# Kernel tuning notes

Measured on AMD Instinct MI355X. Metric: run time of the kernel, lower is better.

## Reference

```python
import jax, jax.numpy as jnp
import numpy as np
import math

B, N, D, H = 2, 64, 256, 8
DK = D // H


def setup_inputs() -> dict:
    key = jax.random.key(0)
    ks = jax.random.split(key, 12)
    s = 1.0 / math.sqrt(D)
    inp = {
        "state": jax.random.normal(ks[0], (B, N, N, D), dtype=jnp.float32),
        "mask": jnp.zeros((B, N, N, N), dtype=bool),
        "W_lk": jax.random.normal(ks[1], (D, D), dtype=jnp.float32) * s,
        "b_lk": jnp.zeros((D,), dtype=jnp.float32),
        "W_rk": jax.random.normal(ks[2], (D, D), dtype=jnp.float32) * s,
        "b_rk": jnp.zeros((D,), dtype=jnp.float32),
        "W_lv": jax.random.normal(ks[3], (D, D), dtype=jnp.float32) * s,
        "b_lv": jnp.zeros((D,), dtype=jnp.float32),
        "W_rv": jax.random.normal(ks[4], (D, D), dtype=jnp.float32) * s,
        "b_rv": jnp.zeros((D,), dtype=jnp.float32),
        "W_o": jax.random.normal(ks[5], (D, D), dtype=jnp.float32) * s,
        "b_o": jnp.zeros((D,), dtype=jnp.float32),
    }
    return inp


def _proj(x, W, b):
    # torch nn.Linear: x @ W.T + b, then view to heads
    y = jnp.einsum('bxyd,ed->bxye', x, W) + b
    return y.reshape(B, N, N, H, DK)


def reference(state, mask, W_lk, b_lk, W_rk, b_rk, W_lv, b_lv, W_rv, b_rv, W_o, b_o):
    left_k = _proj(state, W_lk, b_lk)   # [B,N,N,H,DK]
    right_k = _proj(state, W_rk, b_rk)
    left_v = _proj(state, W_lv, b_lv)
    right_v = _proj(state, W_rv, b_rv)

    # triangle-style scores over node triples (x, a, y): [B,N,N,N,H]
    scores = jnp.einsum('bxahd,bayhd->bxayh', left_k, right_k) / math.sqrt(DK)
    scores = jnp.where(mask[..., None], jnp.float32(-1000.0), scores)
    att = jax.nn.softmax(scores, axis=2)  # softmax over intermediate node a

    # val[b,x,a,y,h,d] = left_v[b,x,a,h,d] * right_v[b,a,y,h,d] (materialized as in torch)
    val = jnp.einsum('bxahd,bayhd->bxayhd', left_v, right_v)
    x = jnp.einsum('bxayh,bxayhd->bxyhd', att, val)  # sum over a
    x = x.reshape(B, N, N, D)
    return jnp.einsum('bxyd,ed->bxye', x, W_o) + b_o
```

## Files before the change

### kernel.cpp

```cpp
#include <hip/hip_runtime.h>

#define B 2
#define N 64
#define D 256
#define H 8
#define DK 32
#define M (B * N * N)

typedef __attribute__((ext_vector_type(8))) short bf16x8;
typedef __attribute__((ext_vector_type(4))) float f32x4;

#define OFF_LK 0
#define OFF_RK 256
#define OFF_LV 512
#define OFF_RV 768

__device__ __forceinline__ ushort f2b(float f) {
    union { float f; unsigned u; } v; v.f = f;
    unsigned r = v.u + 0x7fffu + ((v.u >> 16) & 1u);
    return (ushort)(r >> 16);
}
__device__ __forceinline__ float b2f(ushort u) {
    union { unsigned u; float f; } v; v.u = ((unsigned)u) << 16; return v.f;
}
__device__ __forceinline__ void cvt8(float4 raw, float* f) {
    const ushort* s = (const ushort*)&raw;
#pragma unroll
    for (int j = 0; j < 8; ++j) f[j] = b2f(s[j]);
}

__device__ __forceinline__ void glds16(const ushort* g, ushort* l) {
    __builtin_amdgcn_global_load_lds(
        (const __attribute__((address_space(1))) unsigned int*)g,
        (__attribute__((address_space(3))) unsigned int*)l, 16, 0, 0);
}

__global__ __launch_bounds__(256) void cast_all(const float* __restrict__ state,
                                                const float* __restrict__ W_lk, const float* __restrict__ W_rk,
                                                const float* __restrict__ W_lv, const float* __restrict__ W_rv,
                                                const float* __restrict__ W_o,
                                                const float* __restrict__ b_lk, const float* __restrict__ b_rk,
                                                const float* __restrict__ b_lv, const float* __restrict__ b_rv,
                                                const float* __restrict__ b_o,
                                                ushort* __restrict__ state_bf,
                                                ushort* __restrict__ Wcat,
                                                float* __restrict__ bias_cat) {
    const int gid = blockIdx.x * 256 + threadIdx.x;
    const float* Ws[5] = {W_lk, W_rk, W_lv, W_rv, W_o};
    const float* bs[5] = {b_lk, b_rk, b_lv, b_rv, b_o};

    if (gid < 1280) bias_cat[gid] = bs[gid >> 8][gid & 255];

    if (gid < 524288) {
        float4 v = *(const float4*)&state[(size_t)gid * 4];
        ushort4 o = {f2b(v.x), f2b(v.y), f2b(v.z), f2b(v.w)};
        *(ushort4*)&state_bf[(size_t)gid * 4] = o;
    } else {
        int u = gid - 524288;
        int row = u >> 6;
        int k4 = (u & 63) * 4;
        const float* W = Ws[row >> 8];
        float4 v = *(const float4*)&W[(size_t)(row & 255) * 256 + k4];
        ushort4 o = {f2b(v.x), f2b(v.y), f2b(v.z), f2b(v.w)};
        *(ushort4*)&Wcat[(size_t)row * 256 + k4] = o;
    }
}

template <int BF16OUT>
__global__ __launch_bounds__(256) void gemm_mfma(const ushort* __restrict__ A,
                                                 const ushort* __restrict__ Bw,
                                                 const float* __restrict__ bias,
                                                 void* __restrict__ Cv, int ldc) {
    __shared__ __align__(16) ushort As[128 * 32];
    __shared__ __align__(16) ushort Bs[128 * 32];
    const int tid = threadIdx.x;
    const int lane = tid & 63;
    const int wave = tid >> 6;
    const int wm = (wave & 1) * 64;
    const int wn = (wave >> 1) * 64;
    const int row0 = blockIdx.x * 128;
    const int col0 = blockIdx.y * 128;

    const int lr = lane >> 2;
    const int lkq = (lane & 3) * 8;

    const ushort* gA0 = A + (size_t)(row0 + wave * 32 + lr) * 256 + lkq;
    const ushort* gA1 = gA0 + 16 * 256;
    const ushort* gB0 = Bw + (size_t)(col0 + wave * 32 + lr) * 256 + lkq;
    const ushort* gB1 = gB0 + 16 * 256;
    ushort* lA0 = &As[(wave * 32) * 32];
    ushort* lA1 = &As[(wave * 32 + 16) * 32];
    ushort* lB0 = &Bs[(wave * 32) * 32];
    ushort* lB1 = &Bs[(wave * 32 + 16) * 32];

    const int fr = lane & 15;
    const int fk = (lane >> 4) * 8;

    f32x4 acc[4][4] = {};

    for (int k0 = 0; k0 < 256; k0 += 32) {
        __syncthreads();
        glds16(gA0 + k0, lA0);
        glds16(gA1 + k0, lA1);
        glds16(gB0 + k0, lB0);
        glds16(gB1 + k0, lB1);
        __syncthreads();

        bf16x8 af[4], bf[4];
#pragma unroll
        for (int i = 0; i < 4; ++i)
            af[i] = *(const bf16x8*)&As[(wm + i * 16 + fr) * 32 + fk];
#pragma unroll
        for (int j = 0; j < 4; ++j)
            bf[j] = *(const bf16x8*)&Bs[(wn + j * 16 + fr) * 32 + fk];
#pragma unroll
        for (int i = 0; i < 4; ++i)
#pragma unroll
            for (int j = 0; j < 4; ++j)
                acc[i][j] = __builtin_amdgcn_mfma_f32_16x16x32_bf16(af[i], bf[j], acc[i][j], 0, 0, 0);
    }

#pragma unroll
    for (int j = 0; j < 4; ++j) {
        const int col = col0 + wn + j * 16 + (lane & 15);
        const float bv = bias[col];
#pragma unroll
        for (int i = 0; i < 4; ++i) {
            const int rbase = row0 + wm + i * 16 + (lane >> 4) * 4;
#pragma unroll
            for (int r = 0; r < 4; ++r) {
                float o = acc[i][j][r] + bv;
                if (BF16OUT) ((ushort*)Cv)[(size_t)(rbase + r) * ldc + col] = f2b(o);
                else ((float*)Cv)[(size_t)(rbase + r) * ldc + col] = o;
            }
        }
    }
}

__global__ __launch_bounds__(256) void fused_attn(const ushort* __restrict__ P,
                                                  const unsigned char* __restrict__ mask,
                                                  ushort* __restrict__ xbuf) {
    __shared__ __align__(16) ushort LKs[8 * 16 * 40];
    __shared__ __align__(16) ushort RKs[8 * 16 * 40];
    __shared__ __align__(16) float2 LVs[8 * 16 * 18];
    __shared__ __align__(16) float2 RVs[8 * 16 * 18];
    __shared__ __align__(16) float atts[8 * 16 * 20];
    __shared__ __align__(16) unsigned char masks[16 * 8 * 16];
    __shared__ float mstate[16 * 20];
    __shared__ float lstate[16 * 20];
    __shared__ float alphas[16 * 20];

    const int bh = blockIdx.z;
    const int b = bh >> 3, h = bh & 7;
    const int x0 = blockIdx.x * 16, y0 = blockIdx.y * 16;
    const int tid = threadIdx.x;
    const int lane = tid & 63, wave = tid >> 6;

    const int xg = tid >> 6, yg = (tid >> 4) & 3, dp = tid & 15;
    const int sx = tid >> 4, sy = tid & 15;

    mstate[sx * 20 + sy] = -3.0e38f;
    lstate[sx * 20 + sy] = 0.0f;

    float2 acc[4][4] = {};
    const float scale = 0.17677669529663687f;

    for (int ac = 0; ac < N; ac += 8) {
        __syncthreads();
        {
            const int r = tid >> 1, q = tid & 1;
            const int xs = r >> 3, as = r & 7;
            const int ar = r >> 4, yr = r & 15;
            {
                const ushort* s = &P[(((size_t)b * N + x0 + xs) * N + ac + as) * 1024 + OFF_LK + h * DK + q * 16];
                *(float4*)&LKs[(as * 16 + xs) * 40 + q * 16]     = *(const float4*)&s[0];
                *(float4*)&LKs[(as * 16 + xs) * 40 + q * 16 + 8] = *(const float4*)&s[8];
            }
            {
                const ushort* s = &P[(((size_t)b * N + ac + ar) * N + y0 + yr) * 1024 + OFF_RK + h * DK + q * 16];
                *(float4*)&RKs[(ar * 16 + yr) * 40 + q * 16]     = *(const float4*)&s[0];
                *(float4*)&RKs[(ar * 16 + yr) * 40 + q * 16 + 8] = *(const float4*)&s[8];
            }
            float f[16];
            {
                const ushort* s = &P[(((size_t)b * N + x0 + xs) * N + ac + as) * 1024 + OFF_LV + h * DK + q * 16];
                cvt8(*(const float4*)&s[0], f);
                cvt8(*(const float4*)&s[8], f + 8);
#pragma unroll
                for (int m2 = 0; m2 < 8; ++m2)
                    LVs[(as * 16 + q * 8 + m2) * 18 + xs] = make_float2(f[2 * m2], f[2 * m2 + 1]);
            }
            {
                const ushort* s = &P[(((size_t)b * N + ac + ar) * N + y0 + yr) * 1024 + OFF_RV + h * DK + q * 16];
                cvt8(*(const float4*)&s[0], f);
                cvt8(*(const float4*)&s[8], f + 8);
#pragma unroll
                for (int m2 = 0; m2 < 8; ++m2)
                    RVs[(ar * 16 + q * 8 + m2) * 18 + yr] = make_float2(f[2 * m2], f[2 * m2 + 1]);
            }
            if (tid < 128) {
                const int xm = tid >> 3, am = tid & 7;
                const unsigned char* s = &mask[(((size_t)b * N + x0 + xm) * N + ac + am) * N + y0];
                *(int4*)&masks[(xm * 8 + am) * 16] = *(const int4*)s;
            }
        }
        __syncthreads();

        {
            const int fr = lane & 15;
            const int fkq = (lane >> 4) * 8;
            const int yq = lane & 15, xq = (lane >> 4) * 4;
#pragma unroll
            for (int aw = 0; aw < 2; ++aw) {
                const int a = wave * 2 + aw;
                bf16x8 af = *(const bf16x8*)&LKs[(a * 16 + fr) * 40 + fkq];
                bf16x8 bfv = *(const bf16x8*)&RKs[(a * 16 + fr) * 40 + fkq];
                f32x4 s = {};
                s = __builtin_amdgcn_mfma_f32_16x16x32_bf16(af, bfv, s, 0, 0, 0);
#pragma unroll
                for (int rr = 0; rr < 4; ++rr) {
                    const int x = xq + rr;
                    float sv = s[rr] * scale;
                    if (masks[(x * 8 + a) * 16 + yq]) sv = -1000.0f;
                    atts[(a * 16 + x) * 20 + yq] = sv;
                }
            }
        }
        __syncthreads();

        {
            float s8[8];
#pragma unroll
            for (int a = 0; a < 8; ++a) s8[a] = atts[(a * 16 + sx) * 20 + sy];
            float mc = s8[0];
#pragma unroll
            for (int a = 1; a < 8; ++a) mc = fmaxf(mc, s8[a]);
            const float mold = mstate[sx * 20 + sy];
            const float mnew = fmaxf(mold, mc);
            const float alpha = __expf(mold - mnew);
            float ps = 0.0f;
#pragma unroll
            for (int a = 0; a < 8; ++a) {
                float p = __expf(s8[a] - mnew);
                atts[(a * 16 + sx) * 20 + sy] = p;
                ps += p;
            }
            lstate[sx * 20 + sy] = lstate[sx * 20 + sy] * alpha + ps;
            mstate[sx * 20 + sy] = mnew;
            alphas[sx * 20 + sy] = alpha;
        }
        __syncthreads();

        {
#pragma unroll
            for (int i = 0; i < 4; ++i) {
                float4 av = *(const float4*)&alphas[(xg * 4 + i) * 20 + yg * 4];
                const float* ap = (const float*)&av;
#pragma unroll
                for (int j = 0; j < 4; ++j) {
                    acc[i][j].x *= ap[j];
                    acc[i][j].y *= ap[j];
                }
            }
#pragma unroll
            for (int a = 0; a < 8; ++a) {
                float4 lq0 = *(const float4*)&LVs[(a * 16 + dp) * 18 + xg * 4];
                float4 lq1 = *(const float4*)&LVs[(a * 16 + dp) * 18 + xg * 4 + 2];
                float4 rq0 = *(const float4*)&RVs[(a * 16 + dp) * 18 + yg * 4];
                float4 rq1 = *(const float4*)&RVs[(a * 16 + dp) * 18 + yg * 4 + 2];
                float2 lv[4] = {make_float2(lq0.x, lq0.y), make_float2(lq0.z, lq0.w),
                                make_float2(lq1.x, lq1.y), make_float2(lq1.z, lq1.w)};
                float2 rv[4] = {make_float2(rq0.x, rq0.y), make_float2(rq0.z, rq0.w),
                                make_float2(rq1.x, rq1.y), make_float2(rq1.z, rq1.w)};
#pragma unroll
                for (int i = 0; i < 4; ++i) {
                    float4 at = *(const float4*)&atts[(a * 16 + xg * 4 + i) * 20 + yg * 4];
                    const float* wp = (const float*)&at;
#pragma unroll
                    for (int j = 0; j < 4; ++j) {
                        acc[i][j].x += (wp[j] * lv[i].x) * rv[j].x;
                        acc[i][j].y += (wp[j] * lv[i].y) * rv[j].y;
                    }
                }
            }
        }
    }

#pragma unroll
    for (int i = 0; i < 4; ++i) {
        float4 lq = *(const float4*)&lstate[(xg * 4 + i) * 20 + yg * 4];
        const float* lp = (const float*)&lq;
#pragma unroll
        for (int j = 0; j < 4; ++j) {
            const float invl = 1.0f / lp[j];
            ushort2 o = {f2b(acc[i][j].x * invl), f2b(acc[i][j].y * invl)};
            *(ushort2*)&xbuf[(((size_t)b * N + x0 + xg * 4 + i) * N + y0 + yg * 4 + j) * D + h * DK + 2 * dp] = o;
        }
    }
}

extern "C" void kernel_launch(void* const* d_in, const int* in_sizes, int n_in,
                              void* d_out, int out_size, void* d_ws, size_t ws_size,
                              hipStream_t stream) {
    const float* state = (const float*)d_in[0];
    const unsigned char* mask = (const unsigned char*)d_in[1];
    const float* W_lk = (const float*)d_in[2];
    const float* b_lk = (const float*)d_in[3];
    const float* W_rk = (const float*)d_in[4];
    const float* b_rk = (const float*)d_in[5];
    const float* W_lv = (const float*)d_in[6];
    const float* b_lv = (const float*)d_in[7];
    const float* W_rv = (const float*)d_in[8];
    const float* b_rv = (const float*)d_in[9];
    const float* W_o = (const float*)d_in[10];
    const float* b_o = (const float*)d_in[11];
    float* out = (float*)d_out;

    char* ws = (char*)d_ws;
    ushort* P_bf = (ushort*)ws;
    ws += (size_t)M * 1024 * 2;
    float* bias_cat = (float*)ws;
    ws += 1280 * 4;
    ushort* state_bf = (ushort*)ws;
    ws += (size_t)M * D * 2;
    ushort* Wcat = (ushort*)ws;
    ws += (size_t)1280 * 256 * 2;
    ushort* xbuf_bf = (ushort*)ws;

    cast_all<<<2368, 256, 0, stream>>>(state, W_lk, W_rk, W_lv, W_rv, W_o,
                                       b_lk, b_rk, b_lv, b_rv, b_o,
                                       state_bf, Wcat, bias_cat);
    gemm_mfma<1><<<dim3(M / 128, 8), 256, 0, stream>>>(state_bf, Wcat, bias_cat, P_bf, 1024);
    fused_attn<<<dim3(4, 4, B * H), 256, 0, stream>>>(P_bf, mask, xbuf_bf);
    gemm_mfma<0><<<dim3(M / 128, 2), 256, 0, stream>>>(xbuf_bf, Wcat + 1024 * 256, bias_cat + 1024, out, 256);
}
```

Measured before the change: 133.7 us.

## Restructure fused attention to 512 threads, 16-wide a-chunks and direct LDS loads

The fused attention kernel now launches 512 threads per block and processes 16 intermediate nodes per chunk instead of 8, which halves the number of chunk iterations and barriers. Each thread owns a 2x4 accumulator tile instead of 4x4. The K tiles are loaded with a global-to-LDS helper (glds16), and the V tiles are stored in a d-major padded layout. The intent is more waves per block for latency hiding and fewer synchronisations, at the cost of more LDS per block and half the threads sitting idle during the softmax step.

After: 127.1 us. 4.9% less time.

```diff
diff --git a/kernel.cpp b/kernel.cpp
--- a/kernel.cpp
+++ b/kernel.cpp
@@ -137,15 +137,15 @@
     }
 }
 
-__global__ __launch_bounds__(256) void fused_attn(const ushort* __restrict__ P,
+__global__ __launch_bounds__(512) void fused_attn(const ushort* __restrict__ P,
                                                   const unsigned char* __restrict__ mask,
                                                   ushort* __restrict__ xbuf) {
-    __shared__ __align__(16) ushort LKs[8 * 16 * 40];
-    __shared__ __align__(16) ushort RKs[8 * 16 * 40];
-    __shared__ __align__(16) float2 LVs[8 * 16 * 18];
-    __shared__ __align__(16) float2 RVs[8 * 16 * 18];
-    __shared__ __align__(16) float atts[8 * 16 * 20];
-    __shared__ __align__(16) unsigned char masks[16 * 8 * 16];
+    __shared__ __align__(16) ushort LKs[16 * 16 * 32];
+    __shared__ __align__(16) ushort RKs[16 * 16 * 32];
+    __shared__ __align__(16) float LVs[16 * 16 * 44];
+    __shared__ __align__(16) float RVs[16 * 16 * 44];
+    __shared__ __align__(16) float atts[16 * 16 * 20];
+    __shared__ __align__(16) unsigned char masks[16 * 16 * 16];
     __shared__ float mstate[16 * 20];
     __shared__ float lstate[16 * 20];
     __shared__ float alphas[16 * 20];
@@ -156,92 +156,86 @@
     const int tid = threadIdx.x;
     const int lane = tid & 63, wave = tid >> 6;
 
-    const int xg = tid >> 6, yg = (tid >> 4) & 3, dp = tid & 15;
+    const int y2 = (tid >> 4) & 3, dp = tid & 15;
     const int sx = tid >> 4, sy = tid & 15;
-
-    mstate[sx * 20 + sy] = -3.0e38f;
-    lstate[sx * 20 + sy] = 0.0f;
-
-    float2 acc[4][4] = {};
+    if (tid < 256) {
+        mstate[sx * 20 + sy] = -3.0e38f;
+        lstate[sx * 20 + sy] = 0.0f;
+    }
+
+    float2 acc[2][4] = {};
     const float scale = 0.17677669529663687f;
 
-    for (int ac = 0; ac < N; ac += 8) {
+    for (int ac = 0; ac < N; ac += 16) {
         __syncthreads();
         {
-            const int r = tid >> 1, q = tid & 1;
-            const int xs = r >> 3, as = r & 7;
-            const int ar = r >> 4, yr = r & 15;
-            {
-                const ushort* s = &P[(((size_t)b * N + x0 + xs) * N + ac + as) * 1024 + OFF_LK + h * DK + q * 16];
-                *(float4*)&LKs[(as * 16 + xs) * 40 + q * 16]     = *(const float4*)&s[0];
-                *(float4*)&LKs[(as * 16 + xs) * 40 + q * 16 + 8] = *(const float4*)&s[8];
-            }
-            {
-                const ushort* s = &P[(((size_t)b * N + ac + ar) * N + y0 + yr) * 1024 + OFF_RK + h * DK + q * 16];
-                *(float4*)&RKs[(ar * 16 + yr) * 40 + q * 16]     = *(const float4*)&s[0];
-                *(float4*)&RKs[(ar * 16 + yr) * 40 + q * 16 + 8] = *(const float4*)&s[8];
-            }
-            float f[16];
-            {
-                const ushort* s = &P[(((size_t)b * N + x0 + xs) * N + ac + as) * 1024 + OFF_LV + h * DK + q * 16];
-                cvt8(*(const float4*)&s[0], f);
-                cvt8(*(const float4*)&s[8], f + 8);
-#pragma unroll
-                for (int m2 = 0; m2 < 8; ++m2)
-                    LVs[(as * 16 + q * 8 + m2) * 18 + xs] = make_float2(f[2 * m2], f[2 * m2 + 1]);
-            }
-            {
-                const ushort* s = &P[(((size_t)b * N + ac + ar) * N + y0 + yr) * 1024 + OFF_RV + h * DK + q * 16];
-                cvt8(*(const float4*)&s[0], f);
-                cvt8(*(const float4*)&s[8], f + 8);
-#pragma unroll
-                for (int m2 = 0; m2 < 8; ++m2)
-                    RVs[(ar * 16 + q * 8 + m2) * 18 + yr] = make_float2(f[2 * m2], f[2 * m2 + 1]);
-            }
-            if (tid < 128) {
-                const int xm = tid >> 3, am = tid & 7;
-                const unsigned char* s = &mask[(((size_t)b * N + x0 + xm) * N + ac + am) * N + y0];
-                *(int4*)&masks[(xm * 8 + am) * 16] = *(const int4*)s;
-            }
-        }
-        __syncthreads();
-
-        {
-            const int fr = lane & 15;
-            const int fkq = (lane >> 4) * 8;
-            const int yq = lane & 15, xq = (lane >> 4) * 4;
+            const int xl = lane >> 2;
+            const int qb = (lane & 3) * 8;
 #pragma unroll
             for (int aw = 0; aw < 2; ++aw) {
                 const int a = wave * 2 + aw;
-                bf16x8 af = *(const bf16x8*)&LKs[(a * 16 + fr) * 40 + fkq];
-                bf16x8 bfv = *(const bf16x8*)&RKs[(a * 16 + fr) * 40 + fkq];
+                glds16(&P[(((size_t)b * N + x0 + xl) * N + ac + a) * 1024 + OFF_LK + h * DK + qb],
+                       &LKs[a * 16 * 32]);
+                glds16(&P[(((size_t)b * N + ac + a) * N + y0 + xl) * 1024 + OFF_RK + h * DK + qb],
+                       &RKs[a * 16 * 32]);
+            }
+#pragma unroll
+            for (int it = 0; it < 2; ++it) {
+                const int row = (tid >> 2) + it * 128;
+                const int q = tid & 3;
+                const int a = row >> 4, r = row & 15;
+                float f[8];
+                cvt8(*(const float4*)&P[(((size_t)b * N + x0 + r) * N + ac + a) * 1024 + OFF_LV + h * DK + q * 8], f);
+                *(float4*)&LVs[row * 44 + q * 8]     = make_float4(f[0], f[1], f[2], f[3]);
+                *(float4*)&LVs[row * 44 + q * 8 + 4] = make_float4(f[4], f[5], f[6], f[7]);
+                cvt8(*(const float4*)&P[(((size_t)b * N + ac + a) * N + y0 + r) * 1024 + OFF_RV + h * DK + q * 8], f);
+                *(float4*)&RVs[row * 44 + q * 8]     = make_float4(f[0], f[1], f[2], f[3]);
+                *(float4*)&RVs[row * 44 + q * 8 + 4] = make_float4(f[4], f[5], f[6], f[7]);
+            }
+            if (tid < 256) {
+                const int xm = tid >> 4, am = tid & 15;
+                *(int4*)&masks[(xm * 16 + am) * 16] =
+                    *(const int4*)&mask[(((size_t)b * N + x0 + xm) * N + ac + am) * N + y0];
+            }
+        }
+        __syncthreads();
+
+        {
+            const int fr = lane & 15, fk = (lane >> 4) * 8;
+            const int yq = lane & 15, xq = (lane >> 4) * 4;
+#pragma unroll
+            for (int aw = 0; aw < 2; ++aw) {
+                const int a = wave * 2 + aw;
+                bf16x8 af = *(const bf16x8*)&LKs[(a * 16 + fr) * 32 + fk];
+                bf16x8 bf = *(const bf16x8*)&RKs[(a * 16 + fr) * 32 + fk];
                 f32x4 s = {};
-                s = __builtin_amdgcn_mfma_f32_16x16x32_bf16(af, bfv, s, 0, 0, 0);
+                s = __builtin_amdgcn_mfma_f32_16x16x32_bf16(af, bf, s, 0, 0, 0);
 #pragma unroll
                 for (int rr = 0; rr < 4; ++rr) {
                     const int x = xq + rr;
                     float sv = s[rr] * scale;
-                    if (masks[(x * 8 + a) * 16 + yq]) sv = -1000.0f;
+                    if (masks[(x * 16 + a) * 16 + yq]) sv = -1000.0f;
                     atts[(a * 16 + x) * 20 + yq] = sv;
                 }
             }
         }
         __syncthreads();
 
-        {
-            float s8[8];
-#pragma unroll
-            for (int a = 0; a < 8; ++a) s8[a] = atts[(a * 16 + sx) * 20 + sy];
-            float mc = s8[0];
-#pragma unroll
-            for (int a = 1; a < 8; ++a) mc = fmaxf(mc, s8[a]);
+        if (tid < 256) {
+            float s16[16];
+            float mc = -3.0e38f;
+#pragma unroll
+            for (int a = 0; a < 16; ++a) {
+                s16[a] = atts[(a * 16 + sx) * 20 + sy];
+                mc = fmaxf(mc, s16[a]);
+            }
             const float mold = mstate[sx * 20 + sy];
             const float mnew = fmaxf(mold, mc);
             const float alpha = __expf(mold - mnew);
             float ps = 0.0f;
 #pragma unroll
-            for (int a = 0; a < 8; ++a) {
-                float p = __expf(s8[a] - mnew);
+            for (int a = 0; a < 16; ++a) {
+                float p = __expf(s16[a] - mnew);
                 atts[(a * 16 + sx) * 20 + sy] = p;
                 ps += p;
             }
@@ -251,50 +245,49 @@
         }
         __syncthreads();
 
-        {
-#pragma unroll
-            for (int i = 0; i < 4; ++i) {
-                float4 av = *(const float4*)&alphas[(xg * 4 + i) * 20 + yg * 4];
-                const float* ap = (const float*)&av;
+#pragma unroll
+        for (int i = 0; i < 2; ++i) {
+            const int x = wave * 2 + i;
+            float4 av = *(const float4*)&alphas[x * 20 + y2 * 4];
+            const float* ap = (const float*)&av;
+#pragma unroll
+            for (int j = 0; j < 4; ++j) {
+                acc[i][j].x *= ap[j];
+                acc[i][j].y *= ap[j];
+            }
+        }
+#pragma unroll
+        for (int a = 0; a < 16; ++a) {
+            float2 lv[2], rv[4];
+#pragma unroll
+            for (int i = 0; i < 2; ++i)
+                lv[i] = *(const float2*)&LVs[(a * 16 + wave * 2 + i) * 44 + dp * 2];
+#pragma unroll
+            for (int j = 0; j < 4; ++j)
+                rv[j] = *(const float2*)&RVs[(a * 16 + y2 * 4 + j) * 44 + dp * 2];
+#pragma unroll
+            for (int i = 0; i < 2; ++i) {
+                float4 wv = *(const float4*)&atts[(a * 16 + wave * 2 + i) * 20 + y2 * 4];
+                const float* wp = (const float*)&wv;
 #pragma unroll
                 for (int j = 0; j < 4; ++j) {
-                    acc[i][j].x *= ap[j];
-                    acc[i][j].y *= ap[j];
+                    acc[i][j].x += (wp[j] * lv[i].x) * rv[j].x;
+                    acc[i][j].y += (wp[j] * lv[i].y) * rv[j].y;
                 }
             }
-#pragma unroll
-            for (int a = 0; a < 8; ++a) {
-                float4 lq0 = *(const float4*)&LVs[(a * 16 + dp) * 18 + xg * 4];
-                float4 lq1 = *(const float4*)&LVs[(a * 16 + dp) * 18 + xg * 4 + 2];
-                float4 rq0 = *(const float4*)&RVs[(a * 16 + dp) * 18 + yg * 4];
-                float4 rq1 = *(const float4*)&RVs[(a * 16 + dp) * 18 + yg * 4 + 2];
-                float2 lv[4] = {make_float2(lq0.x, lq0.y), make_float2(lq0.z, lq0.w),
-                                make_float2(lq1.x, lq1.y), make_float2(lq1.z, lq1.w)};
-                float2 rv[4] = {make_float2(rq0.x, rq0.y), make_float2(rq0.z, rq0.w),
-                                make_float2(rq1.x, rq1.y), make_float2(rq1.z, rq1.w)};
-#pragma unroll
-                for (int i = 0; i < 4; ++i) {
-                    float4 at = *(const float4*)&atts[(a * 16 + xg * 4 + i) * 20 + yg * 4];
-                    const float* wp = (const float*)&at;
-#pragma unroll
-                    for (int j = 0; j < 4; ++j) {
-                        acc[i][j].x += (wp[j] * lv[i].x) * rv[j].x;
-                        acc[i][j].y += (wp[j] * lv[i].y) * rv[j].y;
-                    }
-                }
-            }
-        }
-    }
-
-#pragma unroll
-    for (int i = 0; i < 4; ++i) {
-        float4 lq = *(const float4*)&lstate[(xg * 4 + i) * 20 + yg * 4];
+        }
+    }
+
+#pragma unroll
+    for (int i = 0; i < 2; ++i) {
+        const int x = wave * 2 + i;
+        float4 lq = *(const float4*)&lstate[x * 20 + y2 * 4];
         const float* lp = (const float*)&lq;
 #pragma unroll
         for (int j = 0; j < 4; ++j) {
-            const float invl = 1.0f / lp[j];
-            ushort2 o = {f2b(acc[i][j].x * invl), f2b(acc[i][j].y * invl)};
-            *(ushort2*)&xbuf[(((size_t)b * N + x0 + xg * 4 + i) * N + y0 + yg * 4 + j) * D + h * DK + 2 * dp] = o;
+            const float il = 1.0f / lp[j];
+            ushort2 o = {f2b(acc[i][j].x * il), f2b(acc[i][j].y * il)};
+            *(ushort2*)&xbuf[(((size_t)b * N + x0 + x) * N + y0 + y2 * 4 + j) * D + h * DK + 2 * dp] = o;
         }
     }
 }
@@ -331,6 +324,6 @@
                                        b_lk, b_rk, b_lv, b_rv, b_o,
                                        state_bf, Wcat, bias_cat);
     gemm_mfma<1><<<dim3(M / 128, 8), 256, 0, stream>>>(state_bf, Wcat, bias_cat, P_bf, 1024);
-    fused_attn<<<dim3(4, 4, B * H), 256, 0, stream>>>(P_bf, mask, xbuf_bf);
+    fused_attn<<<dim3(4, 4, B * H), 512, 0, stream>>>(P_bf, mask, xbuf_bf);
     gemm_mfma<0><<<dim3(M / 128, 2), 256, 0, stream>>>(xbuf_bf, Wcat + 1024 * 256, bias_cat + 1024, out, 256);
 }
```
